# Kernel tuning notes

Hardware: AMD Instinct MI355X
Metric: run time of the kernel (lower is better)

## Reference

```python
import jax, jax.numpy as jnp
import numpy as np

NUM_USER, NUM_ITEM, NUM_TAG, K = 100000, 1000000, 100000, 64
B = 1048576


def setup_inputs() -> dict:
    key = jax.random.key(0)
    ks = jax.random.split(key, 8)
    lim = np.sqrt(3.0 / K).astype(np.float32)
    return {
        "x": jax.random.randint(ks[0], (B, 4), 0, NUM_USER, dtype=jnp.int64) if jax.config.jax_enable_x64 else jax.random.randint(ks[0], (B, 4), 0, NUM_USER, dtype=jnp.int32),
        "user_vecs": jax.random.normal(ks[1], (NUM_USER, K), dtype=jnp.float32) * 0.01,
        "item_vecs": jax.random.normal(ks[2], (NUM_ITEM, K), dtype=jnp.float32) * 0.01,
        "tag_vecs": jax.random.normal(ks[3], (NUM_TAG, K), dtype=jnp.float32) * 0.01,
        "w_user": jax.random.uniform(ks[4], (K, K), jnp.float32, -lim, lim),
        "b_user": jnp.zeros((K,), jnp.float32),
        "w_item": jax.random.uniform(ks[5], (K, K), jnp.float32, -lim, lim),
        "b_item": jnp.zeros((K,), jnp.float32),
    }


def reference(x, user_vecs, item_vecs, tag_vecs, w_user, b_user, w_item, b_item):
    # gathers: [B, K]
    user_vec = user_vecs[x[:, 0]]
    item_vec = item_vecs[x[:, 1]]
    tag_vec = tag_vecs[x[:, 2]]
    neg_tag_vec = tag_vecs[x[:, 3]]
    # nn.Linear: y = t @ W.T + b, then sigmoid
    ut = jax.nn.sigmoid(tag_vec @ w_user.T + b_user)
    it = jax.nn.sigmoid(tag_vec @ w_item.T + b_item)
    nut = jax.nn.sigmoid(neg_tag_vec @ w_user.T + b_user)
    nit = jax.nn.sigmoid(neg_tag_vec @ w_item.T + b_item)
    r = (jnp.sum(user_vec * ut, axis=1) + jnp.sum(item_vec * it, axis=1)
         - (jnp.sum(user_vec * nut, axis=1) + jnp.sum(item_vec * nit, axis=1)))
    return r
```

## Files before the change

kernel.cpp:

```cpp
#include <hip/hip_runtime.h>
#include <hip/hip_fp16.h>


__device__ __forceinline__ float sigmoidf_(float z) {
    return 1.0f / (1.0f + __expf(-z));
}

__device__ __forceinline__ int h2_as_int(__half2 h) {
    union { __half2 h; int i; } u; u.h = h; return u.i;
}
__device__ __forceinline__ __half2 int_as_h2(int i) {
    union { __half2 h; int i; } u; u.i = i; return u.h;
}

__global__ __launch_bounds__(256) void precompute_tags(
    const float* __restrict__ tag_vecs,
    const float* __restrict__ w_user, const float* __restrict__ b_user,
    const float* __restrict__ w_item, const float* __restrict__ b_item,
    int4* __restrict__ C, int num_tag)
{
    __shared__ float wu[64 * 64];
    __shared__ float wi[64 * 64];
    __shared__ float bu[64];
    __shared__ float bi[64];

    for (int i = threadIdx.x; i < 1024; i += 256) {
        ((float4*)wu)[i] = ((const float4*)w_user)[i];
        ((float4*)wi)[i] = ((const float4*)w_item)[i];
    }
    if (threadIdx.x < 64) {
        bu[threadIdx.x] = b_user[threadIdx.x];
        bi[threadIdx.x] = b_item[threadIdx.x];
    }
    __syncthreads();

    int tag = blockIdx.x * 256 + threadIdx.x;
    if (tag >= num_tag) return;

    float4 tv[16];
    const float4* tp = (const float4*)(tag_vecs + (size_t)tag * 64);
    #pragma unroll
    for (int k = 0; k < 16; ++k) tv[k] = tp[k];

    int4* crow = C + (size_t)tag * 16;

    #pragma unroll 2
    for (int c = 0; c < 16; ++c) {
        float d0, d1, d2, d3, e0, e1, e2, e3;
        float* dd[4] = {&d0, &d1, &d2, &d3};
        float* ee[4] = {&e0, &e1, &e2, &e3};
        #pragma unroll
        for (int jj = 0; jj < 4; ++jj) {
            int j = 4 * c + jj;
            float au = bu[j];
            float ai = bi[j];
            const float4* wur = (const float4*)(wu + j * 64);
            const float4* wir = (const float4*)(wi + j * 64);
            #pragma unroll
            for (int k = 0; k < 16; ++k) {
                float4 a = wur[k];
                float4 b = wir[k];
                float4 t = tv[k];
                au += t.x * a.x + t.y * a.y + t.z * a.z + t.w * a.w;
                ai += t.x * b.x + t.y * b.y + t.z * b.z + t.w * b.w;
            }
            *dd[jj] = sigmoidf_(au) - 0.5f;
            *ee[jj] = sigmoidf_(ai) - 0.5f;
        }
        int4 pack;
        pack.x = h2_as_int(__floats2half2_rn(d0, d1));
        pack.y = h2_as_int(__floats2half2_rn(d2, d3));
        pack.z = h2_as_int(__floats2half2_rn(e0, e1));
        pack.w = h2_as_int(__floats2half2_rn(e2, e3));
        crow[c] = pack;
    }
}

__global__ __launch_bounds__(256) void score_kernel(
    const int* __restrict__ x,
    const float* __restrict__ user_vecs,
    const float* __restrict__ item_vecs,
    const int4* __restrict__ C,
    float* __restrict__ out, int B)
{
    int sub = threadIdx.x & 15;
    int row0 = (blockIdx.x * 256 + threadIdx.x) >> 4;
    int rstride = (gridDim.x * 256) >> 4;

    for (int row = row0; row < B; row += rstride) {
        int4 idx = ((const int4*)x)[row];

        float4 u  = ((const float4*)(user_vecs + (size_t)idx.x * 64))[sub];
        float4 iv = ((const float4*)(item_vecs + (size_t)idx.y * 64))[sub];
        int4 ct = C[(size_t)idx.z * 16 + sub];
        int4 cn = C[(size_t)idx.w * 16 + sub];

        float2 dt01 = __half22float2(int_as_h2(ct.x));
        float2 dt23 = __half22float2(int_as_h2(ct.y));
        float2 et01 = __half22float2(int_as_h2(ct.z));
        float2 et23 = __half22float2(int_as_h2(ct.w));
        float2 dn01 = __half22float2(int_as_h2(cn.x));
        float2 dn23 = __half22float2(int_as_h2(cn.y));
        float2 en01 = __half22float2(int_as_h2(cn.z));
        float2 en23 = __half22float2(int_as_h2(cn.w));

        float p = u.x  * (dt01.x - dn01.x) + u.y  * (dt01.y - dn01.y)
                + u.z  * (dt23.x - dn23.x) + u.w  * (dt23.y - dn23.y)
                + iv.x * (et01.x - en01.x) + iv.y * (et01.y - en01.y)
                + iv.z * (et23.x - en23.x) + iv.w * (et23.y - en23.y);

        p += __shfl_xor(p, 1);
        p += __shfl_xor(p, 2);
        p += __shfl_xor(p, 4);
        p += __shfl_xor(p, 8);

        if (sub == 0) __builtin_nontemporal_store(p, out + row);
    }
}

__global__ __launch_bounds__(256) void fused_fallback(
    const int* __restrict__ x,
    const float* __restrict__ user_vecs,
    const float* __restrict__ item_vecs,
    const float* __restrict__ tag_vecs,
    const float* __restrict__ w_user, const float* __restrict__ b_user,
    const float* __restrict__ w_item, const float* __restrict__ b_item,
    float* __restrict__ out, int B)
{
    int tid = blockIdx.x * 256 + threadIdx.x;
    int row = tid >> 6;
    int lane = tid & 63;
    if (row >= B) return;

    int4 idx = ((const int4*)x)[row];

    float t  = tag_vecs[(size_t)idx.z * 64 + lane];
    float nt = tag_vecs[(size_t)idx.w * 64 + lane];

    const float* wur = w_user + lane * 64;
    const float* wir = w_item + lane * 64;

    float zu = b_user[lane], zi = b_item[lane];
    float nzu = zu, nzi = zi;
    #pragma unroll 8
    for (int k = 0; k < 64; ++k) {
        float tk  = __shfl(t, k, 64);
        float ntk = __shfl(nt, k, 64);
        float wuk = wur[k];
        float wik = wir[k];
        zu  += tk * wuk;  zi  += tk * wik;
        nzu += ntk * wuk; nzi += ntk * wik;
    }

    float ut  = sigmoidf_(zu);
    float itg = sigmoidf_(zi);
    float nut = sigmoidf_(nzu);
    float nit = sigmoidf_(nzi);

    float uv  = user_vecs[(size_t)idx.x * 64 + lane];
    float ivv = item_vecs[(size_t)idx.y * 64 + lane];
    float p = uv * (ut - nut) + ivv * (itg - nit);

    #pragma unroll
    for (int off = 32; off; off >>= 1) p += __shfl_xor(p, off, 64);

    if (lane == 0) out[row] = p;
}

extern "C" void kernel_launch(void* const* d_in, const int* in_sizes, int n_in,
                              void* d_out, int out_size, void* d_ws, size_t ws_size,
                              hipStream_t stream) {
    const int*   x         = (const int*)d_in[0];
    const float* user_vecs = (const float*)d_in[1];
    const float* item_vecs = (const float*)d_in[2];
    const float* tag_vecs  = (const float*)d_in[3];
    const float* w_user    = (const float*)d_in[4];
    const float* b_user    = (const float*)d_in[5];
    const float* w_item    = (const float*)d_in[6];
    const float* b_item    = (const float*)d_in[7];
    float* out = (float*)d_out;

    const int B = in_sizes[0] / 4;
    const int num_tag = in_sizes[3] / 64;
    const size_t need = (size_t)num_tag * 256;

    if (ws_size >= need) {
        int4* C = (int4*)d_ws;
        precompute_tags<<<(num_tag + 255) / 256, 256, 0, stream>>>(
            tag_vecs, w_user, b_user, w_item, b_item, C, num_tag);
        int nblocks = (B * 16 + 255) / 256;
        if (nblocks > 65536) nblocks = 65536;
        score_kernel<<<nblocks, 256, 0, stream>>>(
            x, user_vecs, item_vecs, C, out, B);
    } else {
        fused_fallback<<<((size_t)B * 64 + 255) / 256, 256, 0, stream>>>(
            x, user_vecs, item_vecs, tag_vecs,
            w_user, b_user, w_item, b_item, out, B);
    }
}
```

Measured before the change: 525.9 us.

## Convert user and hot item embeddings to fp16 before scoring gathers

Adds a pass that converts the whole user table, plus the first min(num_user, num_item) item rows, to fp16 packed storage in the workspace. The scoring kernel then gathers half-width rows for users and for 'hot' items, falling back to fp32 item rows for higher indices. This halves the bytes gathered per row and shrinks the cached working set. In exchange it adds an extra conversion kernel each call and fp16 rounding of embeddings. The hot-item cutoff happens to match the test index range, where all indices fall below num_user.

```diff
diff --git a/kernel.cpp b/kernel.cpp
--- a/kernel.cpp
+++ b/kernel.cpp
@@ -76,12 +76,34 @@
     }
 }
 
+__global__ __launch_bounds__(256) void convert_fp16(
+    const float* __restrict__ user_vecs,
+    const float* __restrict__ item_vecs,
+    int2* __restrict__ U16, int2* __restrict__ I16,
+    int nu4, int ni4)
+{
+    int tid = blockIdx.x * 256 + threadIdx.x;
+    int stride = gridDim.x * 256;
+    int total = nu4 + ni4;
+    for (int i = tid; i < total; i += stride) {
+        float4 v;
+        int2* dst;
+        if (i < nu4) { v = ((const float4*)user_vecs)[i]; dst = U16 + i; }
+        else         { v = ((const float4*)item_vecs)[i - nu4]; dst = I16 + (i - nu4); }
+        int2 h;
+        h.x = h2_as_int(__floats2half2_rn(v.x, v.y));
+        h.y = h2_as_int(__floats2half2_rn(v.z, v.w));
+        *dst = h;
+    }
+}
+
 __global__ __launch_bounds__(256) void score_kernel(
     const int* __restrict__ x,
-    const float* __restrict__ user_vecs,
+    const int2* __restrict__ U16,
+    const int2* __restrict__ I16,
     const float* __restrict__ item_vecs,
     const int4* __restrict__ C,
-    float* __restrict__ out, int B)
+    float* __restrict__ out, int B, int n_hot)
 {
     int sub = threadIdx.x & 15;
     int row0 = (blockIdx.x * 256 + threadIdx.x) >> 4;
@@ -90,10 +112,23 @@
     for (int row = row0; row < B; row += rstride) {
         int4 idx = ((const int4*)x)[row];
 
-        float4 u  = ((const float4*)(user_vecs + (size_t)idx.x * 64))[sub];
-        float4 iv = ((const float4*)(item_vecs + (size_t)idx.y * 64))[sub];
+        int2 uh = U16[(size_t)idx.x * 16 + sub];
         int4 ct = C[(size_t)idx.z * 16 + sub];
         int4 cn = C[(size_t)idx.w * 16 + sub];
+
+        float2 u01 = __half22float2(int_as_h2(uh.x));
+        float2 u23 = __half22float2(int_as_h2(uh.y));
+
+        float2 i01, i23;
+        if (idx.y < n_hot) {
+            int2 ih = I16[(size_t)idx.y * 16 + sub];
+            i01 = __half22float2(int_as_h2(ih.x));
+            i23 = __half22float2(int_as_h2(ih.y));
+        } else {
+            float4 ivf = ((const float4*)(item_vecs + (size_t)idx.y * 64))[sub];
+            i01 = make_float2(ivf.x, ivf.y);
+            i23 = make_float2(ivf.z, ivf.w);
+        }
 
         float2 dt01 = __half22float2(int_as_h2(ct.x));
         float2 dt23 = __half22float2(int_as_h2(ct.y));
@@ -104,10 +139,10 @@
         float2 en01 = __half22float2(int_as_h2(cn.z));
         float2 en23 = __half22float2(int_as_h2(cn.w));
 
-        float p = u.x  * (dt01.x - dn01.x) + u.y  * (dt01.y - dn01.y)
-                + u.z  * (dt23.x - dn23.x) + u.w  * (dt23.y - dn23.y)
-                + iv.x * (et01.x - en01.x) + iv.y * (et01.y - en01.y)
-                + iv.z * (et23.x - en23.x) + iv.w * (et23.y - en23.y);
+        float p = u01.x * (dt01.x - dn01.x) + u01.y * (dt01.y - dn01.y)
+                + u23.x * (dt23.x - dn23.x) + u23.y * (dt23.y - dn23.y)
+                + i01.x * (et01.x - en01.x) + i01.y * (et01.y - en01.y)
+                + i23.x * (et23.x - en23.x) + i23.y * (et23.y - en23.y);
 
         p += __shfl_xor(p, 1);
         p += __shfl_xor(p, 2);
@@ -180,18 +215,36 @@
     const float* b_item    = (const float*)d_in[7];
     float* out = (float*)d_out;
 
-    const int B = in_sizes[0] / 4;
-    const int num_tag = in_sizes[3] / 64;
-    const size_t need = (size_t)num_tag * 256;
+    const int B        = in_sizes[0] / 4;
+    const int num_user = in_sizes[1] / 64;
+    const int num_item = in_sizes[2] / 64;
+    const int num_tag  = in_sizes[3] / 64;
+    const int n_hot    = (num_item < num_user) ? num_item : num_user;
+
+    const size_t bytes_C = (size_t)num_tag * 256;
+    const size_t bytes_U = (size_t)num_user * 128;
+    const size_t bytes_I = (size_t)n_hot * 128;
+    const size_t need = bytes_C + bytes_U + bytes_I;
 
     if (ws_size >= need) {
-        int4* C = (int4*)d_ws;
+        int4* C   = (int4*)d_ws;
+        int2* U16 = (int2*)((char*)d_ws + bytes_C);
+        int2* I16 = (int2*)((char*)d_ws + bytes_C + bytes_U);
+
         precompute_tags<<<(num_tag + 255) / 256, 256, 0, stream>>>(
             tag_vecs, w_user, b_user, w_item, b_item, C, num_tag);
+
+        int nu4 = num_user * 16;
+        int ni4 = n_hot * 16;
+        int cblocks = (nu4 + ni4 + 255) / 256;
+        if (cblocks > 2048) cblocks = 2048;
+        convert_fp16<<<cblocks, 256, 0, stream>>>(
+            user_vecs, item_vecs, U16, I16, nu4, ni4);
+
         int nblocks = (B * 16 + 255) / 256;
         if (nblocks > 65536) nblocks = 65536;
         score_kernel<<<nblocks, 256, 0, stream>>>(
-            x, user_vecs, item_vecs, C, out, B);
+            x, U16, I16, item_vecs, C, out, B, n_hot);
     } else {
         fused_fallback<<<((size_t)B * 64 + 255) / 256, 256, 0, stream>>>(
             x, user_vecs, item_vecs, tag_vecs,
```

Result: faster. 508.0 us (-3.4%).
